# Performance work log

Measured on AMD Instinct MI355X. Metric: run time of the kernel, lower is better.

## Reference

```python
import jax, jax.numpy as jnp
import numpy as np

B, N, D, H = 2, 2048, 768, 12
HD = D // H  # head_dim = 64
SCALE = HD ** -0.5


def setup_inputs() -> dict:
    key = jax.random.key(0)
    ks = jax.random.split(key, 8)
    return {
        "x": jax.random.normal(ks[0], (B, N, D), jnp.float32),
        "masks": jax.random.uniform(ks[1], (B, H, N), jnp.float32),
        "lambda_r": jax.random.uniform(ks[2], (B, H), jnp.float32) * 4.0 + 1.0,
        "theta_r": jax.random.uniform(ks[3], (B, H), jnp.float32),
        "mask_weights": jax.random.uniform(ks[4], (B, H), jnp.float32),
        "qkv_w": jax.random.normal(ks[5], (D, 3 * D), jnp.float32) * (D ** -0.5),
        "qkv_b": jnp.zeros((3 * D,), jnp.float32),
        "proj_w": jax.random.normal(ks[6], (D, D), jnp.float32) * (D ** -0.5),
        "proj_b": jnp.zeros((D,), jnp.float32),
    }


def reference(x, masks, lambda_r, theta_r, mask_weights, qkv_w, qkv_b, proj_w, proj_b):
    # qkv projection: [B,N,3D] -> [3,B,H,N,HD]
    qkv = (x @ qkv_w + qkv_b).reshape(B, N, 3, H, HD).transpose(2, 0, 3, 1, 4)
    q, k, v = qkv[0], qkv[1], qkv[2]
    # raw scores [B,H,N,N]
    attn = jnp.einsum('bhqd,bhkd->bhqk', q, k) * SCALE
    # region gate: sigmoid(lambda * (m_i*m_j - theta)) multiplied into scores pre-softmax
    gate = jax.nn.sigmoid(
        lambda_r[:, :, None, None]
        * (masks[:, :, :, None] * masks[:, :, None, :] - theta_r[:, :, None, None])
    )
    attn = jax.nn.softmax(attn * gate, axis=-1)  # dropout is identity in eval
    out = jnp.einsum('bhqk,bhkd->bqhd', attn, v).reshape(B, N, D)
    # per-head output scaling via mask_weights
    out = out * jnp.repeat(mask_weights, HD, axis=-1)[:, None, :]
    return out @ proj_w + proj_b
```

## Files before the change

### kernel.cpp

```cpp
#include <hip/hip_runtime.h>

typedef unsigned short u16;
typedef unsigned int u32;
typedef __attribute__((ext_vector_type(8))) short short8;
typedef __attribute__((ext_vector_type(4))) float f32x4;

#define NB 2
#define NSEQ 2048
#define DIM 768
#define NH 12
#define HDIM 64

#define LOG2E 1.44269504088896f
#define CFOLD 0.18033688f

#if defined(__has_builtin)
#if __has_builtin(__builtin_amdgcn_exp2f)
#define EXPB(x) __builtin_amdgcn_exp2f(x)
#else
#define EXPB(x) exp2f(x)
#endif
#if __has_builtin(__builtin_amdgcn_rcpf)
#define RCP(x) __builtin_amdgcn_rcpf(x)
#else
#define RCP(x) (1.0f / (x))
#endif
#else
#define EXPB(x) exp2f(x)
#define RCP(x) (1.0f / (x))
#endif

__device__ __forceinline__ u16 f2bf(float x) {
    union { float f; unsigned u; } v; v.f = x;
    unsigned r = v.u + 0x7fffu + ((v.u >> 16) & 1u);
    return (u16)(r >> 16);
}

__device__ __forceinline__ u32 pack_bf16(float a, float b) {
    union { float f; u32 u; } A, B; A.f = a; B.f = b;
    u32 ra = A.u + 0x7fffu + ((A.u >> 16) & 1u);
    u32 rb = B.u + 0x7fffu + ((B.u >> 16) & 1u);
    return __builtin_amdgcn_perm(rb, ra, 0x07060302u);
}

__device__ __forceinline__ u32 pack_rtn(float a, float b) {
    union { float f; u32 u; } A, B; A.f = a; B.f = b;
    return __builtin_amdgcn_perm(B.u + 0x8000u, A.u + 0x8000u, 0x07060302u);
}

__device__ __forceinline__ f32x4 mfma16(short8 a, short8 b, f32x4 c) {
    return __builtin_amdgcn_mfma_f32_16x16x32_bf16(a, b, c, 0, 0, 0);
}

__device__ __forceinline__ void glds16(const u16* g, u16* l) {
    __builtin_amdgcn_global_load_lds((const __attribute__((address_space(1))) u32*)g,
                                     (__attribute__((address_space(3))) u32*)l, 16, 0, 0);
}

__global__ __launch_bounds__(256) void prep(const float* __restrict__ x, u16* __restrict__ xb,
                                            const float* __restrict__ qkv_w, u16* __restrict__ wq,
                                            const float* __restrict__ proj_w, u16* __restrict__ wp) {
    const int t = threadIdx.x;
    int bid = blockIdx.x;
    if (bid < 3072) {
        int i = (bid * 256 + t) * 4;
        float4 v = *(const float4*)(x + i);
        *(uint2*)(xb + i) = make_uint2(pack_bf16(v.x, v.y), pack_bf16(v.z, v.w));
        return;
    }
    const float* in; u16* outp; int rows, cols, bx, by;
    if (bid < 3072 + 1728) {
        bid -= 3072; in = qkv_w; outp = wq; rows = 768; cols = 2304;
        bx = bid % 72; by = bid / 72;
    } else {
        bid -= 4800; in = proj_w; outp = wp; rows = 768; cols = 768;
        bx = bid % 24; by = bid / 24;
    }
    __shared__ float tile[32][33];
    int c0 = bx * 32, r0 = by * 32;
    int tx = t & 31, ty = t >> 5;
    #pragma unroll
    for (int i = 0; i < 32; i += 8)
        tile[ty + i][tx] = in[(size_t)(r0 + ty + i) * cols + c0 + tx];
    __syncthreads();
    #pragma unroll
    for (int i = 0; i < 32; i += 8)
        outp[(size_t)(c0 + ty + i) * rows + r0 + tx] = f2bf(tile[tx][ty + i]);
}

__global__ __launch_bounds__(256) void gemm_qkv(const u16* __restrict__ A,
                                                const u16* __restrict__ BT,
                                                const float* __restrict__ bias,
                                                u16* __restrict__ qo,
                                                u16* __restrict__ ko,
                                                u16* __restrict__ vo) {
    __shared__ __align__(16) u16 pool[17408];
    const int bm = blockIdx.y * 128, bn = blockIdx.x * 128;
    const int t = threadIdx.x;
    const int lane = t & 63, wave = t >> 6;
    const int l15 = lane & 15, quad = lane >> 4;
    const int wm = (wave >> 1) * 64, wn = (wave & 1) * 64;

    const int srow = t >> 2;
    const int sc = (t & 3) ^ ((srow >> 1) & 3);
    const u16* ga = A + (size_t)(bm + srow) * DIM + sc * 8;
    const u16* gb = BT + (size_t)(bn + srow) * DIM + sc * 8;
    const int ldst = wave * 512;
    const int swz = (quad ^ ((l15 >> 1) & 3)) * 8;
    u16* As0 = pool;
    u16* Bs0 = pool + 8192;

    f32x4 acc[4][4] = {};
    glds16(ga, As0 + ldst); glds16(ga + (size_t)64 * DIM, As0 + 2048 + ldst);
    glds16(gb, Bs0 + ldst); glds16(gb + (size_t)64 * DIM, Bs0 + 2048 + ldst);
    ga += 32; gb += 32;

    const int NKT = DIM / 32;
    for (int kt = 0; kt < NKT; kt++) {
        const int bo = (kt & 1) * 4096;
        __syncthreads();
        if (kt + 1 < NKT) {
            const int bn2 = (bo ^ 4096);
            glds16(ga, As0 + bn2 + ldst); glds16(ga + (size_t)64 * DIM, As0 + bn2 + 2048 + ldst);
            glds16(gb, Bs0 + bn2 + ldst); glds16(gb + (size_t)64 * DIM, Bs0 + bn2 + 2048 + ldst);
            ga += 32; gb += 32;
        }
        short8 af[4], bf[4];
        #pragma unroll
        for (int i = 0; i < 4; i++) af[i] = *(const short8*)&As0[bo + (wm + i * 16 + l15) * 32 + swz];
        #pragma unroll
        for (int j = 0; j < 4; j++) bf[j] = *(const short8*)&Bs0[bo + (wn + j * 16 + l15) * 32 + swz];
        #pragma unroll
        for (int i = 0; i < 4; i++)
            #pragma unroll
            for (int j = 0; j < 4; j++)
                acc[i][j] = mfma16(af[i], bf[j], acc[i][j]);
    }

    __syncthreads();
    u16* Cs = pool;
    #pragma unroll
    for (int i = 0; i < 4; i++) {
        int row0 = wm + i * 16 + quad * 4;
        #pragma unroll
        for (int j = 0; j < 4; j++) {
            int lcol = wn + j * 16 + l15;
            float bb = bias[bn + lcol];
            #pragma unroll
            for (int r = 0; r < 4; r++)
                Cs[(row0 + r) * 136 + lcol] = f2bf(acc[i][j][r] + bb);
        }
    }
    __syncthreads();

    const int w = bn / DIM;
    const int h0 = (bn - w * DIM) >> 6;
    const int b = bm >> 11, nnb = bm & 2047;
    if (w < 2) {
        u16* dst = w ? ko : qo;
        #pragma unroll
        for (int p = 0; p < 8; p++) {
            int row = p * 16 + (t >> 4);
            int chunk = t & 15;
            short8 v = *(const short8*)&Cs[row * 136 + chunk * 8];
            *(short8*)&dst[(((size_t)(b * NH + h0 + (chunk >> 3))) * NSEQ + nnb + row) * HDIM +
                           (chunk & 7) * 8] = v;
        }
    } else {
        #pragma unroll
        for (int p = 0; p < 8; p++) {
            int hdf = p * 16 + (t >> 4);
            int nn0 = (t & 15) * 8;
            short8 v;
            #pragma unroll
            for (int k = 0; k < 8; k++) v[k] = (short)Cs[(nn0 + k) * 136 + hdf];
            *(short8*)&vo[(((size_t)(b * NH + h0 + (hdf >> 6))) * HDIM + (hdf & 63)) * NSEQ +
                          nnb + nn0] = v;
        }
    }
}

__global__ __launch_bounds__(512) void attn_kernel(const u16* __restrict__ Q,
                                                   const u16* __restrict__ Kg,
                                                   const u16* __restrict__ Vt,
                                                   const float* __restrict__ masks,
                                                   const float* __restrict__ lambda_r,
                                                   const float* __restrict__ theta_r,
                                                   const float* __restrict__ mask_w,
                                                   u16* __restrict__ AO) {
    const int bh = blockIdx.y;
    const int b = bh / NH, h = bh % NH;
    const int qb = blockIdx.x * 64;
    const int t = threadIdx.x, wave = t >> 6, lane = t & 63;
    const int l15 = lane & 15, quad = lane >> 4;
    const int g = wave >> 1, kh = wave & 1;

    __shared__ __align__(16) u16 pool[16384];
    __shared__ __align__(16) u16 Ps[8][640];
    __shared__ __align__(16) float mks[2][64];
    __shared__ float Ls[8][16];

    const float lam = lambda_r[bh], th = theta_r[bh], mw = mask_w[bh];
    const float Bfac = lam * th * LOG2E;

    const size_t base = (size_t)bh * (NSEQ * HDIM);
    const int qrow = qb + g * 16;

    const u16* Qr = Q + base + (size_t)(qrow + l15) * HDIM;
    short8 bq0 = *(const short8*)(Qr + quad * 8);
    short8 bq1 = *(const short8*)(Qr + 32 + quad * 8);
    const float Afac = -lam * LOG2E * masks[bh * NSEQ + qrow + l15];

    const int srow = t >> 3;
    const int gc = (t & 7) ^ (srow & 7);
    const u16* kgp = Kg + base + (size_t)srow * HDIM + gc * 8;
    const u16* vgp = Vt + base + (size_t)srow * NSEQ + gc * 8;
    const int wbase = wave * 512;

    const int ph = (quad ^ (l15 & 7)) * 8;
    const int vph = kh ? (ph ^ 32) : ph;
    u16* PsW = Ps[wave];
    const int pw = l15 * 40 + quad * 4;
    const int prd = l15 * 40 + quad * 8;
    const float* mrow = masks + bh * NSEQ;

    float lsum = 0.f;
    f32x4 O[4] = {};

    glds16(kgp, pool + wbase);
    glds16(vgp, pool + 8192 + wbase);
    if (t < 16) *(float4*)&mks[0][t * 4] = *(const float4*)&mrow[t * 4];

    const int NT = NSEQ / 64;
    for (int kt = 0; kt < NT; kt++) {
        const int bufofs = (kt & 1) * 4096;
        __syncthreads();
        if (kt + 1 < NT) {
            glds16(kgp + (kt + 1) * 64 * HDIM, pool + (bufofs ^ 4096) + wbase);
            glds16(vgp + (kt + 1) * 64, pool + 8192 + (bufofs ^ 4096) + wbase);
            if (t < 16) *(float4*)&mks[(kt + 1) & 1][t * 4] =
                *(const float4*)&mrow[(kt + 1) * 64 + t * 4];
        }
        const u16* KsB = pool + bufofs;
        const u16* VsB = pool + 8192 + bufofs;
        const float* mkb = mks[kt & 1];

        float gp[2][4];
        #pragma unroll
        for (int c = 0; c < 2; c++) {
            float4 mkv = *(const float4*)&mkb[kh * 32 + c * 16 + quad * 4];
            #pragma unroll
            for (int r = 0; r < 4; r++) {
                float mk = (r == 0) ? mkv.x : (r == 1) ? mkv.y : (r == 2) ? mkv.z : mkv.w;
                float e = EXPB(fmaf(mk, Afac, Bfac));
                gp[c][r] = CFOLD * RCP(1.0f + e);
            }
        }

        #pragma unroll
        for (int c = 0; c < 2; c++) {
            const int krow = kh * 32 + c * 16 + l15;
            short8 ak0 = *(const short8*)&KsB[krow * 64 + ph];
            short8 ak1 = *(const short8*)&KsB[krow * 64 + (ph ^ 32)];
            f32x4 S = {0.f, 0.f, 0.f, 0.f};
            S = mfma16(ak0, bq0, S);
            S = mfma16(ak1, bq1, S);
            float p[4];
            #pragma unroll
            for (int r = 0; r < 4; r++) p[r] = EXPB(S[r] * gp[c][r]);
            lsum += (p[0] + p[1]) + (p[2] + p[3]);
            *(uint2*)&PsW[pw + c * 16] = make_uint2(pack_rtn(p[0], p[1]), pack_rtn(p[2], p[3]));
        }

        short8 bp = *(const short8*)&PsW[prd];
        #pragma unroll
        for (int dt = 0; dt < 4; dt++) {
            short8 av = *(const short8*)&VsB[(dt * 16 + l15) * 64 + vph];
            O[dt] = mfma16(av, bp, O[dt]);
        }
    }

    __syncthreads();
    float* Op = (float*)pool;
    const int slot = (wave * 64 + lane) * 16;
    #pragma unroll
    for (int dt = 0; dt < 4; dt++) *(f32x4*)&Op[slot + dt * 4] = O[dt];
    float ls = lsum;
    ls += __shfl_xor(ls, 16);
    ls += __shfl_xor(ls, 32);
    if (quad == 0) Ls[wave][l15] = ls;
    __syncthreads();
    if (kh == 0) {
        const int pslot = ((wave ^ 1) * 64 + lane) * 16;
        float sc = mw / (ls + Ls[wave ^ 1][l15]);
        u16* aor = AO + ((size_t)(b * NSEQ) + qrow + l15) * DIM + h * HDIM + quad * 4;
        #pragma unroll
        for (int dt = 0; dt < 4; dt++) {
            f32x4 oc = *(const f32x4*)&Op[pslot + dt * 4];
            float o0 = (O[dt][0] + oc[0]) * sc, o1 = (O[dt][1] + oc[1]) * sc;
            float o2 = (O[dt][2] + oc[2]) * sc, o3 = (O[dt][3] + oc[3]) * sc;
            *(uint2*)(aor + dt * 16) = make_uint2(pack_rtn(o0, o1), pack_rtn(o2, o3));
        }
    }
}

__global__ __launch_bounds__(256) void gemm_proj(const u16* __restrict__ A,
                                                 const u16* __restrict__ BT,
                                                 const float* __restrict__ bias,
                                                 float* __restrict__ outp) {
    __shared__ __align__(16) u16 As[2][4096];
    __shared__ __align__(16) u16 Bs[2][2048];
    const int bm = blockIdx.y * 128, bn = blockIdx.x * 64;
    const int t = threadIdx.x;
    const int lane = t & 63, wave = t >> 6;
    const int l15 = lane & 15, quad = lane >> 4;
    const int wm = wave * 32;

    const int srow = t >> 2;
    const int sc = (t & 3) ^ ((srow >> 1) & 3);
    const u16* ga = A + (size_t)(bm + srow) * DIM + sc * 8;
    const u16* gb = BT + (size_t)(bn + srow) * DIM + sc * 8;
    const int ldst = wave * 512;
    const int swz = (quad ^ ((l15 >> 1) & 3)) * 8;

    f32x4 acc[2][4] = {};
    glds16(ga, &As[0][ldst]); glds16(ga + (size_t)64 * DIM, &As[0][2048 + ldst]);
    glds16(gb, &Bs[0][ldst]);
    ga += 32; gb += 32;

    const int NKT = DIM / 32;
    for (int kt = 0; kt < NKT; kt++) {
        const int buf = kt & 1;
        __syncthreads();
        if (kt + 1 < NKT) {
            glds16(ga, &As[buf ^ 1][ldst]); glds16(ga + (size_t)64 * DIM, &As[buf ^ 1][2048 + ldst]);
            glds16(gb, &Bs[buf ^ 1][ldst]);
            ga += 32; gb += 32;
        }
        short8 af[2], bf[4];
        #pragma unroll
        for (int i = 0; i < 2; i++) af[i] = *(const short8*)&As[buf][(wm + i * 16 + l15) * 32 + swz];
        #pragma unroll
        for (int j = 0; j < 4; j++) bf[j] = *(const short8*)&Bs[buf][(j * 16 + l15) * 32 + swz];
        #pragma unroll
        for (int i = 0; i < 2; i++)
            #pragma unroll
            for (int j = 0; j < 4; j++)
                acc[i][j] = mfma16(af[i], bf[j], acc[i][j]);
    }

    #pragma unroll
    for (int i = 0; i < 2; i++) {
        int mr = bm + wm + i * 16 + quad * 4;
        #pragma unroll
        for (int j = 0; j < 4; j++) {
            int ncol = bn + j * 16 + l15;
            float bb = bias[ncol];
            #pragma unroll
            for (int r = 0; r < 4; r++)
                outp[(size_t)(mr + r) * DIM + ncol] = acc[i][j][r] + bb;
        }
    }
}

extern "C" void kernel_launch(void* const* d_in, const int* in_sizes, int n_in,
                              void* d_out, int out_size, void* d_ws, size_t ws_size,
                              hipStream_t stream) {
    const float* x            = (const float*)d_in[0];
    const float* masks        = (const float*)d_in[1];
    const float* lambda_r     = (const float*)d_in[2];
    const float* theta_r      = (const float*)d_in[3];
    const float* mask_weights = (const float*)d_in[4];
    const float* qkv_w        = (const float*)d_in[5];
    const float* qkv_b        = (const float*)d_in[6];
    const float* proj_w       = (const float*)d_in[7];
    const float* proj_b       = (const float*)d_in[8];
    float* outp = (float*)d_out;

    const size_t SZH = (size_t)NB * NH * NSEQ * HDIM;
    u16* xb    = (u16*)d_ws;
    u16* wqkvT = xb + (size_t)4096 * 768;
    u16* wprT  = wqkvT + (size_t)2304 * 768;
    u16* qg    = wprT + (size_t)768 * 768;
    u16* kg    = qg + SZH;
    u16* vt    = kg + SZH;
    u16* ao    = xb;

    prep<<<dim3(3072 + 1728 + 576), 256, 0, stream>>>(x, xb, qkv_w, wqkvT, proj_w, wprT);
    gemm_qkv<<<dim3(2304 / 128, 4096 / 128), 256, 0, stream>>>(xb, wqkvT, qkv_b, qg, kg, vt);
    attn_kernel<<<dim3(NSEQ / 64, NB * NH), 512, 0, stream>>>(qg, kg, vt, masks, lambda_r,
                                                              theta_r, mask_weights, ao);
    gemm_proj<<<dim3(768 / 64, 4096 / 128), 256, 0, stream>>>(ao, wprT, proj_b, outp);
}
```

Before: 186.6 us.

## Restructure attention waves to keep P in registers and split keys four ways

The attention kernel now gives each wave 32 query rows and one quarter (16 keys) of each 64-key tile, instead of 16 query rows and half the keys. P is fed straight from registers into 16x16x16 bf16 MFMAs, removing the per-wave LDS staging buffer and its round trip. The mask-gate sigmoid for the next tile is prefetched from global memory and computed ahead of time. The softmax scale is folded into Q in the QKV GEMM epilogue, and a hardware pack-to-bf16 instruction is used when available. In exchange, the final reduction across four key-split waves costs extra LDS passes and barriers, and the occupancy hint in the launch bounds changes.

```diff
diff --git a/kernel.cpp b/kernel.cpp
--- a/kernel.cpp
+++ b/kernel.cpp
@@ -3,6 +3,7 @@
 typedef unsigned short u16;
 typedef unsigned int u32;
 typedef __attribute__((ext_vector_type(8))) short short8;
+typedef __attribute__((ext_vector_type(4))) short short4v;
 typedef __attribute__((ext_vector_type(4))) float f32x4;
 
 #define NB 2
@@ -48,8 +49,22 @@
     return __builtin_amdgcn_perm(B.u + 0x8000u, A.u + 0x8000u, 0x07060302u);
 }
 
+#if defined(__has_builtin) && __has_builtin(__builtin_amdgcn_cvt_pk_bf16_f32)
+__device__ __forceinline__ u32 pkbf(float a, float b) {
+    auto r = __builtin_amdgcn_cvt_pk_bf16_f32(a, b);
+    union { __typeof__(r) v; u32 u; } c; c.v = r;
+    return c.u;
+}
+#else
+#define pkbf pack_rtn
+#endif
+
 __device__ __forceinline__ f32x4 mfma16(short8 a, short8 b, f32x4 c) {
     return __builtin_amdgcn_mfma_f32_16x16x32_bf16(a, b, c, 0, 0, 0);
+}
+
+__device__ __forceinline__ f32x4 mfma1k(short4v a, short4v b, f32x4 c) {
+    return __builtin_amdgcn_mfma_f32_16x16x16bf16_1k(a, b, c, 0, 0, 0);
 }
 
 __device__ __forceinline__ void glds16(const u16* g, u16* l) {
@@ -139,6 +154,8 @@
 
     __syncthreads();
     u16* Cs = pool;
+    const int w = bn / DIM;
+    const float cscale = (w == 0) ? CFOLD : 1.0f;
     #pragma unroll
     for (int i = 0; i < 4; i++) {
         int row0 = wm + i * 16 + quad * 4;
@@ -148,12 +165,11 @@
             float bb = bias[bn + lcol];
             #pragma unroll
             for (int r = 0; r < 4; r++)
-                Cs[(row0 + r) * 136 + lcol] = f2bf(acc[i][j][r] + bb);
+                Cs[(row0 + r) * 136 + lcol] = f2bf((acc[i][j][r] + bb) * cscale);
         }
     }
     __syncthreads();
 
-    const int w = bn / DIM;
     const int h0 = (bn - w * DIM) >> 6;
     const int b = bm >> 11, nnb = bm & 2047;
     if (w < 2) {
@@ -180,36 +196,40 @@
     }
 }
 
-__global__ __launch_bounds__(512) void attn_kernel(const u16* __restrict__ Q,
-                                                   const u16* __restrict__ Kg,
-                                                   const u16* __restrict__ Vt,
-                                                   const float* __restrict__ masks,
-                                                   const float* __restrict__ lambda_r,
-                                                   const float* __restrict__ theta_r,
-                                                   const float* __restrict__ mask_w,
-                                                   u16* __restrict__ AO) {
+__global__ __launch_bounds__(512, 6) void attn_kernel(const u16* __restrict__ Q,
+                                                      const u16* __restrict__ Kg,
+                                                      const u16* __restrict__ Vt,
+                                                      const float* __restrict__ masks,
+                                                      const float* __restrict__ lambda_r,
+                                                      const float* __restrict__ theta_r,
+                                                      const float* __restrict__ mask_w,
+                                                      u16* __restrict__ AO) {
     const int bh = blockIdx.y;
     const int b = bh / NH, h = bh % NH;
     const int qb = blockIdx.x * 64;
     const int t = threadIdx.x, wave = t >> 6, lane = t & 63;
     const int l15 = lane & 15, quad = lane >> 4;
-    const int g = wave >> 1, kh = wave & 1;
+    const int qh = wave >> 2, kh = wave & 3;
 
     __shared__ __align__(16) u16 pool[16384];
-    __shared__ __align__(16) u16 Ps[8][640];
-    __shared__ __align__(16) float mks[2][64];
-    __shared__ float Ls[8][16];
+    __shared__ float Ls[8][2][16];
 
     const float lam = lambda_r[bh], th = theta_r[bh], mw = mask_w[bh];
     const float Bfac = lam * th * LOG2E;
 
     const size_t base = (size_t)bh * (NSEQ * HDIM);
-    const int qrow = qb + g * 16;
-
-    const u16* Qr = Q + base + (size_t)(qrow + l15) * HDIM;
-    short8 bq0 = *(const short8*)(Qr + quad * 8);
-    short8 bq1 = *(const short8*)(Qr + 32 + quad * 8);
-    const float Afac = -lam * LOG2E * masks[bh * NSEQ + qrow + l15];
+    const int qrow = qb + qh * 32;
+
+    short8 bq[2][2];
+    float Afac[2], lsum[2] = {0.f, 0.f};
+    #pragma unroll
+    for (int g = 0; g < 2; g++) {
+        const u16* Qr = Q + base + (size_t)(qrow + g * 16 + l15) * HDIM;
+        bq[g][0] = *(const short8*)(Qr + quad * 8);
+        bq[g][1] = *(const short8*)(Qr + 32 + quad * 8);
+        Afac[g] = -lam * LOG2E * masks[bh * NSEQ + qrow + g * 16 + l15];
+    }
+    f32x4 O[2][4] = {};
 
     const int srow = t >> 3;
     const int gc = (t & 7) ^ (srow & 7);
@@ -217,89 +237,103 @@
     const u16* vgp = Vt + base + (size_t)srow * NSEQ + gc * 8;
     const int wbase = wave * 512;
 
-    const int ph = (quad ^ (l15 & 7)) * 8;
-    const int vph = kh ? (ph ^ 32) : ph;
-    u16* PsW = Ps[wave];
-    const int pw = l15 * 40 + quad * 4;
-    const int prd = l15 * 40 + quad * 8;
+    const int kb0 = (kh * 16 + l15) * 64 + (quad ^ (l15 & 7)) * 8;
+    const int kb1 = kb0 ^ 32;
+    const int voff = l15 * 64 + (((kh * 2 + (quad >> 1)) ^ (l15 & 7)) * 8) + (quad & 1) * 4;
+
     const float* mrow = masks + bh * NSEQ;
-
-    float lsum = 0.f;
-    f32x4 O[4] = {};
 
     glds16(kgp, pool + wbase);
     glds16(vgp, pool + 8192 + wbase);
-    if (t < 16) *(float4*)&mks[0][t * 4] = *(const float4*)&mrow[t * 4];
+    f32x4 mk4 = *(const f32x4*)&mrow[kh * 16 + quad * 4];
+    float gp[2][4];
+    #pragma unroll
+    for (int g = 0; g < 2; g++)
+        #pragma unroll
+        for (int r = 0; r < 4; r++)
+            gp[g][r] = RCP(1.0f + EXPB(fmaf(mk4[r], Afac[g], Bfac)));
 
     const int NT = NSEQ / 64;
     for (int kt = 0; kt < NT; kt++) {
-        const int bufofs = (kt & 1) * 4096;
+        const int bo = (kt & 1) * 4096;
         __syncthreads();
-        if (kt + 1 < NT) {
-            glds16(kgp + (kt + 1) * 64 * HDIM, pool + (bufofs ^ 4096) + wbase);
-            glds16(vgp + (kt + 1) * 64, pool + 8192 + (bufofs ^ 4096) + wbase);
-            if (t < 16) *(float4*)&mks[(kt + 1) & 1][t * 4] =
-                *(const float4*)&mrow[(kt + 1) * 64 + t * 4];
-        }
-        const u16* KsB = pool + bufofs;
-        const u16* VsB = pool + 8192 + bufofs;
-        const float* mkb = mks[kt & 1];
-
-        float gp[2][4];
-        #pragma unroll
-        for (int c = 0; c < 2; c++) {
-            float4 mkv = *(const float4*)&mkb[kh * 32 + c * 16 + quad * 4];
-            #pragma unroll
-            for (int r = 0; r < 4; r++) {
-                float mk = (r == 0) ? mkv.x : (r == 1) ? mkv.y : (r == 2) ? mkv.z : mkv.w;
-                float e = EXPB(fmaf(mk, Afac, Bfac));
-                gp[c][r] = CFOLD * RCP(1.0f + e);
+        f32x4 mk4n;
+        const bool more = (kt + 1 < NT);
+        if (more) {
+            glds16(kgp + (kt + 1) * 64 * HDIM, pool + (bo ^ 4096) + wbase);
+            glds16(vgp + (kt + 1) * 64, pool + 8192 + (bo ^ 4096) + wbase);
+            mk4n = *(const f32x4*)&mrow[(kt + 1) * 64 + kh * 16 + quad * 4];
+        }
+        const u16* KsB = pool + bo;
+        const u16* VsB = pool + 8192 + bo;
+
+        short8 ak0 = *(const short8*)&KsB[kb0];
+        short8 ak1 = *(const short8*)&KsB[kb1];
+        f32x4 S0 = {0.f, 0.f, 0.f, 0.f}, S1 = {0.f, 0.f, 0.f, 0.f};
+        S0 = mfma16(ak0, bq[0][0], S0);
+        S1 = mfma16(ak0, bq[1][0], S1);
+        S0 = mfma16(ak1, bq[0][1], S0);
+        S1 = mfma16(ak1, bq[1][1], S1);
+
+        float p0[4], p1[4];
+        #pragma unroll
+        for (int r = 0; r < 4; r++) p0[r] = EXPB(S0[r] * gp[0][r]);
+        #pragma unroll
+        for (int r = 0; r < 4; r++) p1[r] = EXPB(S1[r] * gp[1][r]);
+        lsum[0] += (p0[0] + p0[1]) + (p0[2] + p0[3]);
+        lsum[1] += (p1[0] + p1[1]) + (p1[2] + p1[3]);
+        union { uint2 u; short4v s; } c0, c1;
+        c0.u = make_uint2(pkbf(p0[0], p0[1]), pkbf(p0[2], p0[3]));
+        c1.u = make_uint2(pkbf(p1[0], p1[1]), pkbf(p1[2], p1[3]));
+
+        if (more) {
+            #pragma unroll
+            for (int g = 0; g < 2; g++)
+                #pragma unroll
+                for (int r = 0; r < 4; r++)
+                    gp[g][r] = RCP(1.0f + EXPB(fmaf(mk4n[r], Afac[g], Bfac)));
+        }
+
+        #pragma unroll
+        for (int dt = 0; dt < 4; dt++) {
+            short4v av = *(const short4v*)&VsB[voff + dt * 1024];
+            O[0][dt] = mfma1k(av, c0.s, O[0][dt]);
+            O[1][dt] = mfma1k(av, c1.s, O[1][dt]);
+        }
+    }
+
+    #pragma unroll
+    for (int g = 0; g < 2; g++) {
+        float ls = lsum[g];
+        ls += __shfl_xor(ls, 16);
+        ls += __shfl_xor(ls, 32);
+        lsum[g] = ls;
+        if (quad == 0 && (lane >> 4) == 0) Ls[wave][g][l15] = ls;
+    }
+    float* Op = (float*)pool;
+    #pragma unroll
+    for (int g = 0; g < 2; g++) {
+        __syncthreads();
+        const int slot = (wave * 64 + lane) * 16;
+        #pragma unroll
+        for (int dt = 0; dt < 4; dt++) *(f32x4*)&Op[slot + dt * 4] = O[g][dt];
+        __syncthreads();
+        if (kh == 0) {
+            float lt = Ls[wave][g][l15] + Ls[wave + 1][g][l15] +
+                       Ls[wave + 2][g][l15] + Ls[wave + 3][g][l15];
+            float sc = mw / lt;
+            u16* aor = AO + ((size_t)(b * NSEQ) + qrow + g * 16 + l15) * DIM + h * HDIM + quad * 4;
+            #pragma unroll
+            for (int dt = 0; dt < 4; dt++) {
+                f32x4 o = O[g][dt];
+                #pragma unroll
+                for (int i = 1; i < 4; i++) {
+                    f32x4 oc = *(const f32x4*)&Op[((wave + i) * 64 + lane) * 16 + dt * 4];
+                    o += oc;
+                }
+                *(uint2*)(aor + dt * 16) = make_uint2(pkbf(o[0] * sc, o[1] * sc),
+                                                      pkbf(o[2] * sc, o[3] * sc));
             }
-        }
-
-        #pragma unroll
-        for (int c = 0; c < 2; c++) {
-            const int krow = kh * 32 + c * 16 + l15;
-            short8 ak0 = *(const short8*)&KsB[krow * 64 + ph];
-            short8 ak1 = *(const short8*)&KsB[krow * 64 + (ph ^ 32)];
-            f32x4 S = {0.f, 0.f, 0.f, 0.f};
-            S = mfma16(ak0, bq0, S);
-            S = mfma16(ak1, bq1, S);
-            float p[4];
-            #pragma unroll
-            for (int r = 0; r < 4; r++) p[r] = EXPB(S[r] * gp[c][r]);
-            lsum += (p[0] + p[1]) + (p[2] + p[3]);
-            *(uint2*)&PsW[pw + c * 16] = make_uint2(pack_rtn(p[0], p[1]), pack_rtn(p[2], p[3]));
-        }
-
-        short8 bp = *(const short8*)&PsW[prd];
-        #pragma unroll
-        for (int dt = 0; dt < 4; dt++) {
-            short8 av = *(const short8*)&VsB[(dt * 16 + l15) * 64 + vph];
-            O[dt] = mfma16(av, bp, O[dt]);
-        }
-    }
-
-    __syncthreads();
-    float* Op = (float*)pool;
-    const int slot = (wave * 64 + lane) * 16;
-    #pragma unroll
-    for (int dt = 0; dt < 4; dt++) *(f32x4*)&Op[slot + dt * 4] = O[dt];
-    float ls = lsum;
-    ls += __shfl_xor(ls, 16);
-    ls += __shfl_xor(ls, 32);
-    if (quad == 0) Ls[wave][l15] = ls;
-    __syncthreads();
-    if (kh == 0) {
-        const int pslot = ((wave ^ 1) * 64 + lane) * 16;
-        float sc = mw / (ls + Ls[wave ^ 1][l15]);
-        u16* aor = AO + ((size_t)(b * NSEQ) + qrow + l15) * DIM + h * HDIM + quad * 4;
-        #pragma unroll
-        for (int dt = 0; dt < 4; dt++) {
-            f32x4 oc = *(const f32x4*)&Op[pslot + dt * 4];
-            float o0 = (O[dt][0] + oc[0]) * sc, o1 = (O[dt][1] + oc[1]) * sc;
-            float o2 = (O[dt][2] + oc[2]) * sc, o3 = (O[dt][3] + oc[3]) * sc;
-            *(uint2*)(aor + dt * 16) = make_uint2(pack_rtn(o0, o1), pack_rtn(o2, o3));
         }
     }
 }
@@ -369,7 +403,7 @@
     const float* x            = (const float*)d_in[0];
     const float* masks        = (const float*)d_in[1];
     const float* lambda_r     = (const float*)d_in[2];
-    const float* theta_r      = (const float*)d_in[3];
+    const float* theta_r     = (const float*)d_in[3];
     const float* mask_weights = (const float*)d_in[4];
     const float* qkv_w        = (const float*)d_in[5];
     const float* qkv_b        = (const float*)d_in[6];
```

After: 234.9 us. 1.26x slower.
